# Kernel tuning notes

Hardware: AMD Instinct MI355X
Metric: run time of the kernel (lower is better)

The kernel has to match this reference:

```python
import jax, jax.numpy as jnp
import numpy as np

GROUPS = 32
EPS = 1e-5
NUM_HEADS = 8
HEAD_DIM = 64
CHANNELS = 512


def group_norm(x, scale, bias):
    # x: [b, h, w, c]; normalize over (h, w, channels-within-group)
    b, h, w, c = x.shape
    xg = x.reshape(b, h, w, GROUPS, c // GROUPS)
    mean = jnp.mean(xg, axis=(1, 2, 4), keepdims=True)
    var = jnp.var(xg, axis=(1, 2, 4), keepdims=True)
    xg = (xg - mean) * jax.lax.rsqrt(var + EPS)
    return xg.reshape(b, h, w, c) * scale + bias


def setup_inputs() -> dict:
    key = jax.random.key(0)
    ks = jax.random.split(key, 8)
    b, hs, ws, c = 8, 32, 32, CHANNELS
    inner = NUM_HEADS * HEAD_DIM
    return {
        "x": jax.random.normal(ks[0], (b, hs, ws, c), dtype=jnp.float32),
        "t": jax.random.normal(ks[1], (b,), dtype=jnp.float32),
        "gn_scale": jnp.ones((c,), dtype=jnp.float32),
        "gn_bias": jnp.zeros((c,), dtype=jnp.float32),
        "w_qkv": jax.random.normal(ks[2], (c, 3 * inner), dtype=jnp.float32) * 0.02,
        "b_qkv": jnp.zeros((3 * inner,), dtype=jnp.float32),
        "w_out": jax.random.normal(ks[3], (inner, c), dtype=jnp.float32) * 0.02,
        "b_out": jnp.zeros((c,), dtype=jnp.float32),
    }


def reference(x, t, gn_scale, gn_bias, w_qkv, b_qkv, w_out, b_out):
    b, hs, ws, c = x.shape
    # NOTE: original reassigns x = GroupNorm(x); the residual uses the NORMALIZED x.
    xn = group_norm(x, gn_scale, gn_bias)
    x_flat = xn.reshape(b, hs * ws, c)                      # [b, s, c]
    qkv = x_flat @ w_qkv + b_qkv                            # [b, s, 3*nh*hd]
    qkv = qkv.reshape(b, hs * ws, NUM_HEADS, 3 * HEAD_DIM)
    q, k, v = jnp.split(qkv, 3, axis=-1)                    # each [b, s, nh, hd]
    q = q / jnp.sqrt(jnp.float32(HEAD_DIM))
    q = q.transpose(0, 2, 1, 3)                             # [b, nh, s, hd]
    k = k.transpose(0, 2, 1, 3)
    v = v.transpose(0, 2, 1, 3)
    attn = jax.nn.softmax(jnp.einsum('bhqd,bhkd->bhqk', q, k), axis=-1)
    out = jnp.einsum('bhqk,bhkd->bhqd', attn, v)            # [b, nh, s, hd]
    out = out.transpose(0, 2, 1, 3).reshape(b, hs * ws, NUM_HEADS * HEAD_DIM)
    h = out @ w_out + b_out                                 # [b, s, c]
    h = h.reshape(b, hs, ws, c)
    return xn + h
```

## Files before the change

kernel.cpp:

```cpp
#include <hip/hip_runtime.h>
#include <hip/hip_bf16.h>


#define B_    8
#define S_    1024
#define C_    512
#define NH    8
#define HD    64
#define QKVC  1536
#define GROUPS 32
#define GSIZE  16
#define EPSV   1e-5f
#define QSCL  0.18033688f

using frag8 = __attribute__((ext_vector_type(8))) short;
using f32x4 = __attribute__((ext_vector_type(4))) float;

__device__ __forceinline__ float bf2f(unsigned short u) {
    union { unsigned int i; float f; } v; v.i = ((unsigned int)u) << 16; return v.f;
}
__device__ __forceinline__ unsigned short f2bf(float f) {
    union { float f; unsigned int i; } v; v.f = f;
    unsigned int x = v.i;
    return (unsigned short)((x + 0x7fffu + ((x >> 16) & 1u)) >> 16);
}
__device__ __forceinline__ unsigned int pk2bf(float a, float b) {
    union { float f; unsigned int u; } x, y; x.f = a; y.f = b;
    return __builtin_amdgcn_perm(y.u + 0x8000u, x.u + 0x8000u, 0x07060302u);
}
__device__ __forceinline__ float fexp2(float x) {
#if __has_builtin(__builtin_amdgcn_exp2f)
    return __builtin_amdgcn_exp2f(x);
#else
    return exp2f(x);
#endif
}
__device__ __forceinline__ f32x4 zero4() {
    f32x4 z; z[0] = 0.f; z[1] = 0.f; z[2] = 0.f; z[3] = 0.f; return z;
}
__device__ __forceinline__ void gl_lds(const unsigned short* gp, unsigned short* lp) {
    __builtin_amdgcn_global_load_lds(
        (const __attribute__((address_space(1))) void*)gp,
        (__attribute__((address_space(3))) void*)lp, 16, 0, 0);
}

__global__ __launch_bounds__(256) void transpose2_kernel(
        const float* __restrict__ w_qkv, const float* __restrict__ w_out,
        unsigned short* __restrict__ wqkvT, unsigned short* __restrict__ woutT) {
    __shared__ float tile[32][33];
    int id = blockIdx.x;
    const float* in; unsigned short* out; int N, n0, k0;
    if (id < 768) { in = w_qkv; out = wqkvT; N = QKVC; n0 = (id % 48) * 32; k0 = (id / 48) * 32; }
    else { id -= 768; in = w_out; out = woutT; N = C_; n0 = (id % 16) * 32; k0 = (id / 16) * 32; }
    int t = threadIdx.x;
    for (int i = 0; i < 4; ++i) {
        int idx = t + i * 256; int r = idx >> 5, c = idx & 31;
        tile[r][c] = in[(size_t)(k0 + r) * N + n0 + c];
    }
    __syncthreads();
    for (int i = 0; i < 4; ++i) {
        int idx = t + i * 256; int r = idx >> 5, c = idx & 31;
        out[(size_t)(n0 + r) * C_ + k0 + c] = f2bf(tile[c][r]);
    }
}

__global__ __launch_bounds__(256) void gn_kernel(
        const float* __restrict__ x,
        const float* __restrict__ scale,
        const float* __restrict__ bias,
        unsigned short* __restrict__ xn) {
    int bg = blockIdx.x;
    int b = bg >> 5, g = bg & 31;
    const float* xb = x + (size_t)b * S_ * C_;
    int t = threadIdx.x;

    float sum = 0.f, ss = 0.f;
    for (int i = 0; i < 16; ++i) {
        int idx = t + i * 256;
        int row = idx >> 2, j = idx & 3;
        float4 v = *(const float4*)(xb + (size_t)row * C_ + g * GSIZE + j * 4);
        sum += v.x + v.y + v.z + v.w;
        ss  += v.x * v.x + v.y * v.y + v.z * v.z + v.w * v.w;
    }
    for (int off = 1; off < 64; off <<= 1) {
        sum += __shfl_xor(sum, off);
        ss  += __shfl_xor(ss,  off);
    }
    __shared__ float s_sum[4], s_ss[4];
    int wid = t >> 6;
    if ((t & 63) == 0) { s_sum[wid] = sum; s_ss[wid] = ss; }
    __syncthreads();
    sum = s_sum[0] + s_sum[1] + s_sum[2] + s_sum[3];
    ss  = s_ss[0]  + s_ss[1]  + s_ss[2]  + s_ss[3];
    float mean = sum * (1.f / 16384.f);
    float var  = ss * (1.f / 16384.f) - mean * mean;
    float rinv = rsqrtf(var + EPSV);

    float sc[16], bi[16];
    for (int u = 0; u < 16; ++u) {
        sc[u] = scale[g * GSIZE + u];
        bi[u] = bias[g * GSIZE + u];
    }
    for (int i = 0; i < 16; ++i) {
        int idx = t + i * 256;
        int row = idx >> 2, j = idx & 3;
        float4 v = *(const float4*)(xb + (size_t)row * C_ + g * GSIZE + j * 4);
        int c0 = j * 4;
        float f0 = (v.x - mean) * rinv * sc[c0 + 0] + bi[c0 + 0];
        float f1 = (v.y - mean) * rinv * sc[c0 + 1] + bi[c0 + 1];
        float f2 = (v.z - mean) * rinv * sc[c0 + 2] + bi[c0 + 2];
        float f3 = (v.w - mean) * rinv * sc[c0 + 3] + bi[c0 + 3];
        uint2 o;
        o.x = (unsigned int)f2bf(f0) | ((unsigned int)f2bf(f1) << 16);
        o.y = (unsigned int)f2bf(f2) | ((unsigned int)f2bf(f3) << 16);
        *(uint2*)(xn + (size_t)b * S_ * C_ + (size_t)row * C_ + g * GSIZE + c0) = o;
    }
}

template<int MODE>
__global__ __launch_bounds__(256) void gemm_kernel(
        const unsigned short* __restrict__ A,
        const unsigned short* __restrict__ Bt,
        const float* __restrict__ bias,
        const unsigned short* __restrict__ resid,
        unsigned short* __restrict__ outA,
        unsigned short* __restrict__ outV,
        float* __restrict__ outF,
        int M, int N, int K) {
    __shared__ unsigned short As[2][128 * 32];
    __shared__ unsigned short Bs[2][128 * 32];
    int m0 = blockIdx.y * 128, n0 = blockIdx.x * 128;
    int t = threadIdx.x;
    int wid = t >> 6, lane = t & 63;
    int quad = lane >> 4, l16 = lane & 15;
    int wm = (wid >> 1) * 64, wn = (wid & 1) * 64;

    f32x4 acc[4][4];
    for (int mi = 0; mi < 4; ++mi)
        for (int ni = 0; ni < 4; ++ni) acc[mi][ni] = zero4();

    int srow = t >> 2, sseg = t & 3;
    auto stage = [&](int k0, int buf) {
        for (int i = 0; i < 2; ++i) {
            gl_lds(A + (size_t)(m0 + i * 64 + srow) * K + k0 + sseg * 8,
                   &As[buf][(size_t)(i * 256 + wid * 64) * 8]);
            gl_lds(Bt + (size_t)(n0 + i * 64 + srow) * K + k0 + sseg * 8,
                   &Bs[buf][(size_t)(i * 256 + wid * 64) * 8]);
        }
    };

    stage(0, 0);
    int nk = K >> 5;
    for (int i = 0; i < nk; ++i) {
        __syncthreads();
        if (i + 1 < nk) stage((i + 1) << 5, (i + 1) & 1);
        int buf = i & 1;

        frag8 bfrag[4], afrag[4];
        for (int ni = 0; ni < 4; ++ni)
            bfrag[ni] = *(const frag8*)(&Bs[buf][(wn + ni * 16 + l16) * 32 + quad * 8]);
        for (int mi = 0; mi < 4; ++mi)
            afrag[mi] = *(const frag8*)(&As[buf][(wm + mi * 16 + l16) * 32 + quad * 8]);

        for (int mi = 0; mi < 4; ++mi)
            for (int ni = 0; ni < 4; ++ni)
                acc[mi][ni] = __builtin_amdgcn_mfma_f32_16x16x32_bf16(
                    afrag[mi], bfrag[ni], acc[mi][ni], 0, 0, 0);
    }

    for (int ni = 0; ni < 4; ++ni) {
        int c0 = n0 + wn + ni * 16;
        float bv = bias[c0 + l16];
        if (MODE == 0) {
            int h = c0 / 192, rr = c0 % 192;
            if (rr >= 128) {
                int d = rr - 128 + l16;
                int bidx = m0 >> 10;
                unsigned short* vp = outV + (((size_t)bidx * NH + h) * HD + d) * S_
                                   + (m0 & 1023) + wm + quad * 4;
                for (int mi = 0; mi < 4; ++mi) {
                    uint2 pk;
                    pk.x = pk2bf(acc[mi][ni][0] + bv, acc[mi][ni][1] + bv);
                    pk.y = pk2bf(acc[mi][ni][2] + bv, acc[mi][ni][3] + bv);
                    *(uint2*)(vp + mi * 16) = pk;
                }
            } else {
                float scl = (rr < 64) ? QSCL : 1.0f;
                int colk = h * 128 + rr + l16;
                for (int mi = 0; mi < 4; ++mi)
                    for (int r = 0; r < 4; ++r) {
                        int row = m0 + wm + mi * 16 + quad * 4 + r;
                        outA[(size_t)row * 1024 + colk] = f2bf((acc[mi][ni][r] + bv) * scl);
                    }
            }
        } else {
            int col = c0 + l16;
            for (int mi = 0; mi < 4; ++mi)
                for (int r = 0; r < 4; ++r) {
                    int row = m0 + wm + mi * 16 + quad * 4 + r;
                    float v = acc[mi][ni][r] + bv + bf2f(resid[(size_t)row * N + col]);
                    outF[(size_t)row * N + col] = v;
                }
        }
    }
}

__global__ __launch_bounds__(256) void attn_kernel(
        const unsigned short* __restrict__ kq,
        const unsigned short* __restrict__ vT,
        unsigned short* __restrict__ attn_out) {
    int i = blockIdx.x;
    int xcd = i & 7, slot = i >> 3;
    int bh = xcd * 8 + (slot >> 4);
    int qt = slot & 15;
    int b = bh >> 3, h = bh & 7;

    int t = threadIdx.x;
    int wid = t >> 6, lane = t & 63, quad = lane >> 4, l16 = lane & 15;
    int q0 = qt * 64 + wid * 16;

    __shared__ unsigned short Ks[2][2048];
    __shared__ unsigned short Vs[2][2048];
    __shared__ unsigned short Ps[4][16 * 40];

    const unsigned short* qrow = kq + ((size_t)b * S_ + q0 + l16) * 1024 + h * 128;
    frag8 qf0 = *(const frag8*)(qrow + quad * 8);
    frag8 qf1 = *(const frag8*)(qrow + 32 + quad * 8);

    frag8 ones;
    for (int i2 = 0; i2 < 8; ++i2) ones[i2] = (short)0x3f80;

    f32x4 o[4], ol;
    ol = zero4();
    for (int dt = 0; dt < 4; ++dt) o[dt] = zero4();

    const unsigned short* kbase = kq + (size_t)b * S_ * 1024 + h * 128 + 64;
    const unsigned short* vbase = vT + ((size_t)b * NH + h) * HD * S_;
    unsigned short* pw = &Ps[wid][0];

    int kdh = wid & 1, krh = wid >> 1;
    int krow = krh * 16 + (lane >> 2);
    int kseg = lane & 3;
    int vd = wid * 16 + (lane >> 2);
    int vseg = lane & 3;

    auto stage = [&](int j0, int buf) {
        gl_lds(kbase + (size_t)(j0 + krow) * 1024 + kdh * 32 + kseg * 8,
               &Ks[buf][kdh * 1024 + krh * 512]);
        gl_lds(vbase + (size_t)vd * S_ + j0 + vseg * 8,
               &Vs[buf][wid * 512]);
    };

    stage(0, 0);

    for (int it = 0; it < S_ / 32; ++it) {
        int cur = it & 1, nxt = cur ^ 1;
        __syncthreads();
        if (it < S_ / 32 - 1) stage((it + 1) * 32, nxt);

        frag8 kf[2][2];
        for (int kh = 0; kh < 2; ++kh)
            for (int dh = 0; dh < 2; ++dh)
                kf[kh][dh] = *(const frag8*)(&Ks[cur][dh * 1024 + (kh * 16 + l16) * 32 + quad * 8]);

        f32x4 s[2];
        for (int kh = 0; kh < 2; ++kh) {
            f32x4 acc = zero4();
            acc = __builtin_amdgcn_mfma_f32_16x16x32_bf16(kf[kh][0], qf0, acc, 0, 0, 0);
            acc = __builtin_amdgcn_mfma_f32_16x16x32_bf16(kf[kh][1], qf1, acc, 0, 0, 0);
            s[kh] = acc;
        }

        for (int kh = 0; kh < 2; ++kh) {
            float p0 = fexp2(s[kh][0]);
            float p1 = fexp2(s[kh][1]);
            float p2 = fexp2(s[kh][2]);
            float p3 = fexp2(s[kh][3]);
            uint2 pk;
            pk.x = pk2bf(p0, p1);
            pk.y = pk2bf(p2, p3);
            *(uint2*)(&pw[l16 * 40 + kh * 16 + quad * 4]) = pk;
        }

        frag8 pf = *(const frag8*)(&pw[l16 * 40 + quad * 8]);

        frag8 vf[4];
        for (int dt = 0; dt < 4; ++dt)
            vf[dt] = *(const frag8*)(&Vs[cur][(dt * 16 + l16) * 32 + quad * 8]);

        ol = __builtin_amdgcn_mfma_f32_16x16x32_bf16(pf, ones, ol, 0, 0, 0);
        for (int dt = 0; dt < 4; ++dt)
            o[dt] = __builtin_amdgcn_mfma_f32_16x16x32_bf16(pf, vf[dt], o[dt], 0, 0, 0);
    }

    for (int r = 0; r < 4; ++r) {
        float inv = 1.0f / ol[r];
        int qrw = q0 + quad * 4 + r;
        for (int dt = 0; dt < 4; ++dt) {
            int ch = h * HD + dt * 16 + l16;
            attn_out[((size_t)b * S_ + qrw) * C_ + ch] = f2bf(o[dt][r] * inv);
        }
    }
}

extern "C" void kernel_launch(void* const* d_in, const int* in_sizes, int n_in,
                              void* d_out, int out_size, void* d_ws, size_t ws_size,
                              hipStream_t stream) {
    const float* x        = (const float*)d_in[0];
    const float* gn_scale = (const float*)d_in[2];
    const float* gn_bias  = (const float*)d_in[3];
    const float* w_qkv    = (const float*)d_in[4];
    const float* b_qkv    = (const float*)d_in[5];
    const float* w_out    = (const float*)d_in[6];
    const float* b_out    = (const float*)d_in[7];
    float* out = (float*)d_out;

    char* ws = (char*)d_ws;
    unsigned short* xn    = (unsigned short*)(ws);
    unsigned short* kq    = (unsigned short*)(ws + ((size_t)8  << 20));
    unsigned short* attn  = (unsigned short*)(ws + ((size_t)24 << 20));
    unsigned short* vT    = (unsigned short*)(ws + ((size_t)32 << 20));
    unsigned short* wqkvT = (unsigned short*)(ws + ((size_t)40 << 20));
    unsigned short* woutT = (unsigned short*)(ws + ((size_t)40 << 20) + ((size_t)3 << 19));

    transpose2_kernel<<<dim3(1024), 256, 0, stream>>>(w_qkv, w_out, wqkvT, woutT);

    gn_kernel<<<dim3(B_ * GROUPS), 256, 0, stream>>>(x, gn_scale, gn_bias, xn);

    gemm_kernel<0><<<dim3(QKVC / 128, (B_ * S_) / 128), 256, 0, stream>>>(
        xn, wqkvT, b_qkv, nullptr, kq, vT, nullptr, B_ * S_, QKVC, C_);

    attn_kernel<<<dim3(1024), 256, 0, stream>>>(kq, vT, attn);

    gemm_kernel<1><<<dim3(C_ / 128, (B_ * S_) / 128), 256, 0, stream>>>(
        attn, woutT, b_out, xn, nullptr, nullptr, out, B_ * S_, C_, C_);
}
```

Measured before the change: 164.8 us.

## Merge weight transpose with groupnorm and keep softmax probabilities in registers

The weight-transpose and groupnorm kernels are merged into one prep launch, so a kernel launch and its inter-kernel gap go away. In attention, the P tile no longer round-trips through LDS. V is instead written into LDS with a permuted column order, so the register layout from the QK^T MFMA output can feed the PV MFMA directly. V now moves through registers with a prefetch-and-write-after-compute pattern instead of direct global-to-LDS loads. This trades extra register pressure and scattered LDS writes for fewer LDS round trips and one fewer launch.

```diff
diff --git a/kernel.cpp b/kernel.cpp
--- a/kernel.cpp
+++ b/kernel.cpp
@@ -44,35 +44,33 @@
         (__attribute__((address_space(3))) void*)lp, 16, 0, 0);
 }
 
-__global__ __launch_bounds__(256) void transpose2_kernel(
+__global__ __launch_bounds__(256) void prep_kernel(
         const float* __restrict__ w_qkv, const float* __restrict__ w_out,
-        unsigned short* __restrict__ wqkvT, unsigned short* __restrict__ woutT) {
+        unsigned short* __restrict__ wqkvT, unsigned short* __restrict__ woutT,
+        const float* __restrict__ x,
+        const float* __restrict__ scale, const float* __restrict__ bias,
+        unsigned short* __restrict__ xn) {
     __shared__ float tile[32][33];
     int id = blockIdx.x;
-    const float* in; unsigned short* out; int N, n0, k0;
-    if (id < 768) { in = w_qkv; out = wqkvT; N = QKVC; n0 = (id % 48) * 32; k0 = (id / 48) * 32; }
-    else { id -= 768; in = w_out; out = woutT; N = C_; n0 = (id % 16) * 32; k0 = (id / 16) * 32; }
     int t = threadIdx.x;
-    for (int i = 0; i < 4; ++i) {
-        int idx = t + i * 256; int r = idx >> 5, c = idx & 31;
-        tile[r][c] = in[(size_t)(k0 + r) * N + n0 + c];
-    }
-    __syncthreads();
-    for (int i = 0; i < 4; ++i) {
-        int idx = t + i * 256; int r = idx >> 5, c = idx & 31;
-        out[(size_t)(n0 + r) * C_ + k0 + c] = f2bf(tile[c][r]);
-    }
-}
-
-__global__ __launch_bounds__(256) void gn_kernel(
-        const float* __restrict__ x,
-        const float* __restrict__ scale,
-        const float* __restrict__ bias,
-        unsigned short* __restrict__ xn) {
-    int bg = blockIdx.x;
+    if (id < 1024) {
+        const float* in; unsigned short* out; int N, n0, k0;
+        if (id < 768) { in = w_qkv; out = wqkvT; N = QKVC; n0 = (id % 48) * 32; k0 = (id / 48) * 32; }
+        else { int i2 = id - 768; in = w_out; out = woutT; N = C_; n0 = (i2 % 16) * 32; k0 = (i2 / 16) * 32; }
+        for (int i = 0; i < 4; ++i) {
+            int idx = t + i * 256; int r = idx >> 5, c = idx & 31;
+            tile[r][c] = in[(size_t)(k0 + r) * N + n0 + c];
+        }
+        __syncthreads();
+        for (int i = 0; i < 4; ++i) {
+            int idx = t + i * 256; int r = idx >> 5, c = idx & 31;
+            out[(size_t)(n0 + r) * C_ + k0 + c] = f2bf(tile[c][r]);
+        }
+        return;
+    }
+    int bg = id - 1024;
     int b = bg >> 5, g = bg & 31;
     const float* xb = x + (size_t)b * S_ * C_;
-    int t = threadIdx.x;
 
     float sum = 0.f, ss = 0.f;
     for (int i = 0; i < 16; ++i) {
@@ -221,7 +219,6 @@
 
     __shared__ unsigned short Ks[2][2048];
     __shared__ unsigned short Vs[2][2048];
-    __shared__ unsigned short Ps[4][16 * 40];
 
     const unsigned short* qrow = kq + ((size_t)b * S_ + q0 + l16) * 1024 + h * 128;
     frag8 qf0 = *(const frag8*)(qrow + quad * 8);
@@ -236,27 +233,42 @@
 
     const unsigned short* kbase = kq + (size_t)b * S_ * 1024 + h * 128 + 64;
     const unsigned short* vbase = vT + ((size_t)b * NH + h) * HD * S_;
-    unsigned short* pw = &Ps[wid][0];
 
     int kdh = wid & 1, krh = wid >> 1;
     int krow = krh * 16 + (lane >> 2);
     int kseg = lane & 3;
     int vd = wid * 16 + (lane >> 2);
     int vseg = lane & 3;
-
-    auto stage = [&](int j0, int buf) {
+    int vkh = vseg >> 1, vsp = vseg & 1;
+    int vbase1 = vsp * 16 + vkh * 4;
+
+    auto stageK = [&](int j0, int buf) {
         gl_lds(kbase + (size_t)(j0 + krow) * 1024 + kdh * 32 + kseg * 8,
                &Ks[buf][kdh * 1024 + krh * 512]);
-        gl_lds(vbase + (size_t)vd * S_ + j0 + vseg * 8,
-               &Vs[buf][wid * 512]);
     };
-
-    stage(0, 0);
+    auto loadV = [&](int j0) {
+        return *(const uint4*)(vbase + (size_t)vd * S_ + j0 + vseg * 8);
+    };
+    auto writeV = [&](uint4 w, int buf) {
+        unsigned short* vdst = &Vs[buf][vd * 32];
+        uint2 g1; g1.x = w.x; g1.y = w.y;
+        uint2 g2; g2.x = w.z; g2.y = w.w;
+        *(uint2*)(vdst + vbase1)     = g1;
+        *(uint2*)(vdst + vbase1 + 8) = g2;
+    };
+
+    stageK(0, 0);
+    writeV(loadV(0), 0);
 
     for (int it = 0; it < S_ / 32; ++it) {
         int cur = it & 1, nxt = cur ^ 1;
         __syncthreads();
-        if (it < S_ / 32 - 1) stage((it + 1) * 32, nxt);
+        uint4 vnext;
+        bool more = (it < S_ / 32 - 1);
+        if (more) {
+            stageK((it + 1) * 32, nxt);
+            vnext = loadV((it + 1) * 32);
+        }
 
         frag8 kf[2][2];
         for (int kh = 0; kh < 2; ++kh)
@@ -271,26 +283,21 @@
             s[kh] = acc;
         }
 
-        for (int kh = 0; kh < 2; ++kh) {
-            float p0 = fexp2(s[kh][0]);
-            float p1 = fexp2(s[kh][1]);
-            float p2 = fexp2(s[kh][2]);
-            float p3 = fexp2(s[kh][3]);
-            uint2 pk;
-            pk.x = pk2bf(p0, p1);
-            pk.y = pk2bf(p2, p3);
-            *(uint2*)(&pw[l16 * 40 + kh * 16 + quad * 4]) = pk;
-        }
-
-        frag8 pf = *(const frag8*)(&pw[l16 * 40 + quad * 8]);
+        union { frag8 f; unsigned int u[4]; } pfu;
+        pfu.u[0] = pk2bf(fexp2(s[0][0]), fexp2(s[0][1]));
+        pfu.u[1] = pk2bf(fexp2(s[0][2]), fexp2(s[0][3]));
+        pfu.u[2] = pk2bf(fexp2(s[1][0]), fexp2(s[1][1]));
+        pfu.u[3] = pk2bf(fexp2(s[1][2]), fexp2(s[1][3]));
 
         frag8 vf[4];
         for (int dt = 0; dt < 4; ++dt)
             vf[dt] = *(const frag8*)(&Vs[cur][(dt * 16 + l16) * 32 + quad * 8]);
 
-        ol = __builtin_amdgcn_mfma_f32_16x16x32_bf16(pf, ones, ol, 0, 0, 0);
+        ol = __builtin_amdgcn_mfma_f32_16x16x32_bf16(pfu.f, ones, ol, 0, 0, 0);
         for (int dt = 0; dt < 4; ++dt)
-            o[dt] = __builtin_amdgcn_mfma_f32_16x16x32_bf16(pf, vf[dt], o[dt], 0, 0, 0);
+            o[dt] = __builtin_amdgcn_mfma_f32_16x16x32_bf16(pfu.f, vf[dt], o[dt], 0, 0, 0);
+
+        if (more) writeV(vnext, nxt);
     }
 
     for (int r = 0; r < 4; ++r) {
@@ -323,9 +330,8 @@
     unsigned short* wqkvT = (unsigned short*)(ws + ((size_t)40 << 20));
     unsigned short* woutT = (unsigned short*)(ws + ((size_t)40 << 20) + ((size_t)3 << 19));
 
-    transpose2_kernel<<<dim3(1024), 256, 0, stream>>>(w_qkv, w_out, wqkvT, woutT);
-
-    gn_kernel<<<dim3(B_ * GROUPS), 256, 0, stream>>>(x, gn_scale, gn_bias, xn);
+    prep_kernel<<<dim3(1280), 256, 0, stream>>>(
+        w_qkv, w_out, wqkvT, woutT, x, gn_scale, gn_bias, xn);
 
     gemm_kernel<0><<<dim3(QKVC / 128, (B_ * S_) / 128), 256, 0, stream>>>(
         xn, wqkvT, b_qkv, nullptr, kq, vT, nullptr, B_ * S_, QKVC, C_);
```

Result: faster. 160.2 us (-2.8%).
